# Kernel optimization log

Measured on AMD Instinct MI355X. Metric: run time of the kernel, lower is better.

The kernel has to match this reference:

```python
import jax, jax.numpy as jnp
import numpy as np

BLOCK_SIZE = 64

def quantize_dequantize(w, block_size=BLOCK_SIZE):
    # LPBQ double quantization: block-wise abs-max -> uint4 scale1 over fp32 scale2
    out_ch, in_ch = w.shape
    pad_len = (block_size - in_ch % block_size) % block_size
    if pad_len > 0:
        w = jnp.pad(w, ((0, 0), (0, pad_len)))
    wr = w.reshape(out_ch, -1, block_size)                      # [O, nB, B]
    s1 = jnp.clip(jnp.max(jnp.abs(wr), axis=-1, keepdims=True) / 7.0, 1e-8)   # [O, nB, 1]
    s2 = jnp.clip(jnp.max(s1, axis=1, keepdims=True) / 15.0, 1e-8)            # [O, 1, 1]
    s1_q = jnp.clip(jnp.round(s1 / s2), 0.0, 15.0)
    s1_recon = s1_q * s2
    w_q = jnp.clip(jnp.round(wr / s1_recon), -8.0, 7.0)
    w_recon = (w_q * s1_recon).reshape(out_ch, -1)
    if pad_len > 0:
        w_recon = w_recon[:, :-pad_len]
    return w_recon

def setup_inputs() -> dict:
    key = jax.random.key(0)
    k1, k2, k3 = jax.random.split(key, 3)
    B, S, IN, OUT = 1, 128, 4096, 11008
    x = jax.random.normal(k1, (B, S, IN), dtype=jnp.float32)
    weight = jax.random.normal(k2, (OUT, IN), dtype=jnp.float32)
    bias = jax.random.normal(k3, (OUT,), dtype=jnp.float32)
    return {"x": x, "weight": weight, "bias": bias}

def reference(x, weight, bias):
    w_q = quantize_dequantize(weight)
    # F.linear: x @ w_q.T + bias
    return jnp.einsum('bsi,oi->bso', x, w_q) + bias
```

## Files before the change

### kernel.cpp

```cpp
#include <hip/hip_runtime.h>
#include <hip/hip_bf16.h>

#define IN_CH 4096
#define OUT_CH 11008
#define QBLK 64

#define BM 128
#define BN 64
#define BK 64
#define KCHUNKS (IN_CH / BK)
#define KSPLIT 4
#define SPLIT_CHUNKS (KCHUNKS / KSPLIT)
#define NTILES (OUT_CH / BN)
#define XCONV_BLOCKS 16
#define BPAD 72

typedef short bf16x8 __attribute__((ext_vector_type(8)));
typedef float f32x4 __attribute__((ext_vector_type(4)));
typedef char char16v __attribute__((ext_vector_type(16)));

#define GLOBAL_AS __attribute__((address_space(1)))
#define LDS_AS __attribute__((address_space(3)))

__device__ inline unsigned short f2bf(float f) {
    union { __hip_bfloat16 h; unsigned short u; } cv;
    cv.h = __float2bfloat16(f);
    return cv.u;
}

__global__ __launch_bounds__(256) void quant_kernel(
        const float* __restrict__ w, const float* __restrict__ x,
        signed char* __restrict__ wq, float* __restrict__ s1rT,
        unsigned short* __restrict__ xq) {
    const int tid = threadIdx.x;

    if (blockIdx.x >= OUT_CH) {
        const int bx = blockIdx.x - OUT_CH;
        for (int it = 0; it < 16; ++it) {
            const int G = it * 4096 + bx * 256 + tid;
            const int row = G >> 9;
            const int gi = G & 511;
            const int kc = gi >> 3;
            const int gp = gi & 7;
            const int gl = gp ^ (row & 7);
            const float4* src =
                (const float4*)(x + (size_t)row * IN_CH + kc * 64 + gl * 8);
            float4 a = src[0], b = src[1];
            ushort4 o0, o1;
            o0.x = f2bf(a.x); o0.y = f2bf(a.y); o0.z = f2bf(a.z); o0.w = f2bf(a.w);
            o1.x = f2bf(b.x); o1.y = f2bf(b.y); o1.z = f2bf(b.z); o1.w = f2bf(b.w);
            ushort4* dst = (ushort4*)(xq + (size_t)row * IN_CH + gi * 8);
            dst[0] = o0;
            dst[1] = o1;
        }
        return;
    }

    const int row = blockIdx.x;
    const float* wrow = w + (size_t)row * IN_CH;
    signed char* orow = wq + (size_t)row * IN_CH;

    __shared__ float s1_lds[64];

    float4 v[4];
    const int lane16 = tid & 15;

    for (int p = 0; p < 4; ++p) {
        v[p] = ((const float4*)wrow)[p * 256 + tid];
        float m = fmaxf(fmaxf(fabsf(v[p].x), fabsf(v[p].y)),
                        fmaxf(fabsf(v[p].z), fabsf(v[p].w)));
        m = fmaxf(m, __shfl_xor(m, 1));
        m = fmaxf(m, __shfl_xor(m, 2));
        m = fmaxf(m, __shfl_xor(m, 4));
        m = fmaxf(m, __shfl_xor(m, 8));
        if (lane16 == 0)
            s1_lds[p * 16 + (tid >> 4)] = fmaxf(m * (1.0f / 7.0f), 1e-8f);
    }
    __syncthreads();

    if (tid < 64) {
        float s1 = s1_lds[tid];
        float m = s1;
        m = fmaxf(m, __shfl_xor(m, 1));
        m = fmaxf(m, __shfl_xor(m, 2));
        m = fmaxf(m, __shfl_xor(m, 4));
        m = fmaxf(m, __shfl_xor(m, 8));
        m = fmaxf(m, __shfl_xor(m, 16));
        m = fmaxf(m, __shfl_xor(m, 32));
        const float s2 = fmaxf(m * (1.0f / 15.0f), 1e-8f);
        const float s1q = fminf(fmaxf(rintf(s1 / s2), 0.0f), 15.0f);
        const float s1r = s1q * s2;
        s1_lds[tid] = s1r;
        s1rT[(size_t)tid * OUT_CH + row] = s1r;
    }
    __syncthreads();

    for (int p = 0; p < 4; ++p) {
        const float s1r = s1_lds[p * 16 + (tid >> 4)];
        char4 o;
        o.x = (signed char)(int)fminf(fmaxf(rintf(v[p].x / s1r), -8.0f), 7.0f);
        o.y = (signed char)(int)fminf(fmaxf(rintf(v[p].y / s1r), -8.0f), 7.0f);
        o.z = (signed char)(int)fminf(fmaxf(rintf(v[p].z / s1r), -8.0f), 7.0f);
        o.w = (signed char)(int)fminf(fmaxf(rintf(v[p].w / s1r), -8.0f), 7.0f);
        ((char4*)orow)[p * 256 + tid] = o;
    }
}

__global__ __launch_bounds__(256) void gemm_kernel(
        const unsigned short* __restrict__ A, const signed char* __restrict__ WQ,
        const float* __restrict__ s1rT, float* __restrict__ part) {
    __shared__ __align__(16) unsigned short ldsA[BM * BK];
    __shared__ __align__(16) unsigned short ldsB[BN * BPAD];

    const int tid = threadIdx.x;
    const int w = tid >> 6;
    const int l = tid & 63;
    const int wm = w >> 1;
    const int wn = w & 1;
    const int n0 = blockIdx.x * BN;
    const int kc0 = blockIdx.y * SPLIT_CHUNKS;

    const int r8 = l >> 3;
    const int sg = l & 7;

    const int brow = tid >> 2;
    const int bcg = tid & 3;

    f32x4 acc[4][2] = {};

    const int lane15 = l & 15;
    const int quad = l >> 4;

    for (int kc = kc0; kc < kc0 + SPLIT_CHUNKS; ++kc) {
        const int k0 = kc * BK;

        for (int i = 0; i < 4; ++i) {
            const unsigned short* gp =
                A + (size_t)(i * 32 + w * 8 + r8) * IN_CH + k0 + sg * 8;
            LDS_AS unsigned short* lp =
                (LDS_AS unsigned short*)&ldsA[(i * 32 + w * 8) * BK];
            __builtin_amdgcn_global_load_lds((const GLOBAL_AS void*)gp,
                                             (LDS_AS void*)lp, 16, 0, 0);
        }

        const float s1 = s1rT[(size_t)kc * OUT_CH + n0 + brow];
        char16v bq = *(const char16v*)(WQ + (size_t)(n0 + brow) * IN_CH +
                                       k0 + bcg * 16);
        bf16x8 o0, o1;
        for (int i = 0; i < 8; ++i)
            o0[i] = (short)f2bf((float)bq[i] * s1);
        for (int i = 0; i < 8; ++i)
            o1[i] = (short)f2bf((float)bq[8 + i] * s1);
        *(bf16x8*)&ldsB[brow * BPAD + bcg * 16] = o0;
        *(bf16x8*)&ldsB[brow * BPAD + bcg * 16 + 8] = o1;

        asm volatile("s_waitcnt vmcnt(0)" ::: "memory");
        __syncthreads();

        for (int kk = 0; kk < 2; ++kk) {
            bf16x8 af[4], bfv[2];
            const int ko = kk * 32 + quad * 8;
            for (int i = 0; i < 4; ++i) {
                const int row = wm * 64 + i * 16 + lane15;
                const int pg = ((kk * 4 + quad) ^ (row & 7)) * 8;
                af[i] = *(const bf16x8*)&ldsA[row * BK + pg];
            }
            for (int j = 0; j < 2; ++j)
                bfv[j] = *(const bf16x8*)&ldsB[(wn * 32 + j * 16 + lane15) * BPAD + ko];
            for (int i = 0; i < 4; ++i)
                for (int j = 0; j < 2; ++j)
                    acc[i][j] = __builtin_amdgcn_mfma_f32_16x16x32_bf16(
                        af[i], bfv[j], acc[i][j], 0, 0, 0);
        }
        __syncthreads();
    }

    float* pbase = part + (size_t)blockIdx.y * BM * OUT_CH;
    const int m_base = wm * 64 + quad * 4;
    const int n_base = n0 + wn * 32 + lane15;
    for (int j = 0; j < 2; ++j) {
        for (int i = 0; i < 4; ++i) {
            const int m = m_base + i * 16;
            float* cp = pbase + (size_t)m * OUT_CH + n_base + j * 16;
            cp[0 * OUT_CH] = acc[i][j][0];
            cp[1 * OUT_CH] = acc[i][j][1];
            cp[2 * OUT_CH] = acc[i][j][2];
            cp[3 * OUT_CH] = acc[i][j][3];
        }
    }
}

__global__ __launch_bounds__(256) void reduce_kernel(
        const float* __restrict__ part, const float* __restrict__ bias,
        float* __restrict__ out) {
    const int m = blockIdx.y;
    const int x4 = blockIdx.x * 256 + threadIdx.x;
    if (x4 >= OUT_CH / 4) return;
    const size_t off = (size_t)m * OUT_CH + x4 * 4;

    float4 acc = ((const float4*)bias)[x4];
    for (int s = 0; s < KSPLIT; ++s) {
        float4 p = *(const float4*)(part + (size_t)s * BM * OUT_CH + off);
        acc.x += p.x; acc.y += p.y; acc.z += p.z; acc.w += p.w;
    }
    *(float4*)(out + off) = acc;
}

extern "C" void kernel_launch(void* const* d_in, const int* in_sizes, int n_in,
                              void* d_out, int out_size, void* d_ws, size_t ws_size,
                              hipStream_t stream) {
    const float* x = (const float*)d_in[0];
    const float* weight = (const float*)d_in[1];
    const float* bias = (const float*)d_in[2];
    float* out = (float*)d_out;

    signed char* wsQ = (signed char*)d_ws;
    unsigned short* wsX = (unsigned short*)(wsQ + (size_t)OUT_CH * IN_CH);
    float* wsS = (float*)(wsX + (size_t)BM * IN_CH);
    float* wsP = wsS + (size_t)QBLK * OUT_CH;

    quant_kernel<<<OUT_CH + XCONV_BLOCKS, 256, 0, stream>>>(weight, x, wsQ, wsS, wsX);
    gemm_kernel<<<dim3(NTILES, KSPLIT), 256, 0, stream>>>(wsX, wsQ, wsS, wsP);
    reduce_kernel<<<dim3((OUT_CH / 4 + 255) / 256, BM), 256, 0, stream>>>(
        wsP, bias, out);
}
```

Baseline: 293.4 us.

## Drop int8 weight workspace; requantize fp32 weights inside GEMM with register prefetch

The first kernel now computes only the per-block scales and the bf16 copy of x; it no longer writes int8 quantized weights. The GEMM reads the original fp32 weights directly, quantizes and dequantizes them to bf16 on the fly using the precomputed scales, and prefetches the next K-chunk into registers while the current MFMA work runs. This removes the 45MB int8 write and its later read-back, but the GEMM now reads 4-byte weights instead of 1-byte and does more ALU work per element, including a divide.

New measurement: 302.4 us. 3.1% more time.

```diff
diff --git a/kernel.cpp b/kernel.cpp
--- a/kernel.cpp
+++ b/kernel.cpp
@@ -17,7 +17,6 @@
 
 typedef short bf16x8 __attribute__((ext_vector_type(8)));
 typedef float f32x4 __attribute__((ext_vector_type(4)));
-typedef char char16v __attribute__((ext_vector_type(16)));
 
 #define GLOBAL_AS __attribute__((address_space(1)))
 #define LDS_AS __attribute__((address_space(3)))
@@ -28,10 +27,16 @@
     return cv.u;
 }
 
-__global__ __launch_bounds__(256) void quant_kernel(
+__device__ inline void dq4(float4 v, float s1, short* o) {
+    o[0] = (short)f2bf(fminf(fmaxf(rintf(v.x / s1), -8.0f), 7.0f) * s1);
+    o[1] = (short)f2bf(fminf(fmaxf(rintf(v.y / s1), -8.0f), 7.0f) * s1);
+    o[2] = (short)f2bf(fminf(fmaxf(rintf(v.z / s1), -8.0f), 7.0f) * s1);
+    o[3] = (short)f2bf(fminf(fmaxf(rintf(v.w / s1), -8.0f), 7.0f) * s1);
+}
+
+__global__ __launch_bounds__(256) void scale_kernel(
         const float* __restrict__ w, const float* __restrict__ x,
-        signed char* __restrict__ wq, float* __restrict__ s1rT,
-        unsigned short* __restrict__ xq) {
+        float* __restrict__ s1rT, unsigned short* __restrict__ xq) {
     const int tid = threadIdx.x;
 
     if (blockIdx.x >= OUT_CH) {
@@ -58,17 +63,14 @@
 
     const int row = blockIdx.x;
     const float* wrow = w + (size_t)row * IN_CH;
-    signed char* orow = wq + (size_t)row * IN_CH;
 
     __shared__ float s1_lds[64];
-
-    float4 v[4];
     const int lane16 = tid & 15;
 
     for (int p = 0; p < 4; ++p) {
-        v[p] = ((const float4*)wrow)[p * 256 + tid];
-        float m = fmaxf(fmaxf(fabsf(v[p].x), fabsf(v[p].y)),
-                        fmaxf(fabsf(v[p].z), fabsf(v[p].w)));
+        float4 v = ((const float4*)wrow)[p * 256 + tid];
+        float m = fmaxf(fmaxf(fabsf(v.x), fabsf(v.y)),
+                        fmaxf(fabsf(v.z), fabsf(v.w)));
         m = fmaxf(m, __shfl_xor(m, 1));
         m = fmaxf(m, __shfl_xor(m, 2));
         m = fmaxf(m, __shfl_xor(m, 4));
@@ -89,25 +91,12 @@
         m = fmaxf(m, __shfl_xor(m, 32));
         const float s2 = fmaxf(m * (1.0f / 15.0f), 1e-8f);
         const float s1q = fminf(fmaxf(rintf(s1 / s2), 0.0f), 15.0f);
-        const float s1r = s1q * s2;
-        s1_lds[tid] = s1r;
-        s1rT[(size_t)tid * OUT_CH + row] = s1r;
-    }
-    __syncthreads();
-
-    for (int p = 0; p < 4; ++p) {
-        const float s1r = s1_lds[p * 16 + (tid >> 4)];
-        char4 o;
-        o.x = (signed char)(int)fminf(fmaxf(rintf(v[p].x / s1r), -8.0f), 7.0f);
-        o.y = (signed char)(int)fminf(fmaxf(rintf(v[p].y / s1r), -8.0f), 7.0f);
-        o.z = (signed char)(int)fminf(fmaxf(rintf(v[p].z / s1r), -8.0f), 7.0f);
-        o.w = (signed char)(int)fminf(fmaxf(rintf(v[p].w / s1r), -8.0f), 7.0f);
-        ((char4*)orow)[p * 256 + tid] = o;
+        s1rT[(size_t)tid * OUT_CH + row] = s1q * s2;
     }
 }
 
 __global__ __launch_bounds__(256) void gemm_kernel(
-        const unsigned short* __restrict__ A, const signed char* __restrict__ WQ,
+        const unsigned short* __restrict__ A, const float* __restrict__ W,
         const float* __restrict__ s1rT, float* __restrict__ part) {
     __shared__ __align__(16) unsigned short ldsA[BM * BK];
     __shared__ __align__(16) unsigned short ldsB[BN * BPAD];
@@ -131,6 +120,13 @@
     const int lane15 = l & 15;
     const int quad = l >> 4;
 
+    const float* wseg = W + (size_t)(n0 + brow) * IN_CH + bcg * 16;
+
+    float4 c0 = ((const float4*)(wseg + kc0 * 64))[0];
+    float4 c1 = ((const float4*)(wseg + kc0 * 64))[1];
+    float4 c2 = ((const float4*)(wseg + kc0 * 64))[2];
+    float4 c3 = ((const float4*)(wseg + kc0 * 64))[3];
+
     for (int kc = kc0; kc < kc0 + SPLIT_CHUNKS; ++kc) {
         const int k0 = kc * BK;
 
@@ -144,18 +140,28 @@
         }
 
         const float s1 = s1rT[(size_t)kc * OUT_CH + n0 + brow];
-        char16v bq = *(const char16v*)(WQ + (size_t)(n0 + brow) * IN_CH +
-                                       k0 + bcg * 16);
-        bf16x8 o0, o1;
-        for (int i = 0; i < 8; ++i)
-            o0[i] = (short)f2bf((float)bq[i] * s1);
-        for (int i = 0; i < 8; ++i)
-            o1[i] = (short)f2bf((float)bq[8 + i] * s1);
-        *(bf16x8*)&ldsB[brow * BPAD + bcg * 16] = o0;
-        *(bf16x8*)&ldsB[brow * BPAD + bcg * 16 + 8] = o1;
+        {
+            bf16x8 ob0, ob1;
+            short t0[4], t1[4], t2[4], t3[4];
+            dq4(c0, s1, t0); dq4(c1, s1, t1); dq4(c2, s1, t2); dq4(c3, s1, t3);
+            ob0[0] = t0[0]; ob0[1] = t0[1]; ob0[2] = t0[2]; ob0[3] = t0[3];
+            ob0[4] = t1[0]; ob0[5] = t1[1]; ob0[6] = t1[2]; ob0[7] = t1[3];
+            ob1[0] = t2[0]; ob1[1] = t2[1]; ob1[2] = t2[2]; ob1[3] = t2[3];
+            ob1[4] = t3[0]; ob1[5] = t3[1]; ob1[6] = t3[2]; ob1[7] = t3[3];
+            *(bf16x8*)&ldsB[brow * BPAD + bcg * 16] = ob0;
+            *(bf16x8*)&ldsB[brow * BPAD + bcg * 16 + 8] = ob1;
+        }
 
         asm volatile("s_waitcnt vmcnt(0)" ::: "memory");
         __syncthreads();
+
+        if (kc + 1 < kc0 + SPLIT_CHUNKS) {
+            const float* np = wseg + (kc + 1) * 64;
+            c0 = ((const float4*)np)[0];
+            c1 = ((const float4*)np)[1];
+            c2 = ((const float4*)np)[2];
+            c3 = ((const float4*)np)[3];
+        }
 
         for (int kk = 0; kk < 2; ++kk) {
             bf16x8 af[4], bfv[2];
@@ -214,13 +220,12 @@
     const float* bias = (const float*)d_in[2];
     float* out = (float*)d_out;
 
-    signed char* wsQ = (signed char*)d_ws;
-    unsigned short* wsX = (unsigned short*)(wsQ + (size_t)OUT_CH * IN_CH);
+    unsigned short* wsX = (unsigned short*)d_ws;
     float* wsS = (float*)(wsX + (size_t)BM * IN_CH);
     float* wsP = wsS + (size_t)QBLK * OUT_CH;
 
-    quant_kernel<<<OUT_CH + XCONV_BLOCKS, 256, 0, stream>>>(weight, x, wsQ, wsS, wsX);
-    gemm_kernel<<<dim3(NTILES, KSPLIT), 256, 0, stream>>>(wsX, wsQ, wsS, wsP);
+    scale_kernel<<<OUT_CH + XCONV_BLOCKS, 256, 0, stream>>>(weight, x, wsS, wsX);
+    gemm_kernel<<<dim3(NTILES, KSPLIT), 256, 0, stream>>>(wsX, weight, wsS, wsP);
     reduce_kernel<<<dim3((OUT_CH / 4 + 255) / 256, BM), 256, 0, stream>>>(
         wsP, bias, out);
 }
```
